# Kernel optimization log

Measured on AMD Instinct MI355X. Metric: run time of the kernel, lower is better.

Reference implementation:

```python
import jax, jax.numpy as jnp
import numpy as np

K_NN = 3
EPS = 1e-8
MASK_THRESH = 0.5


def _three_nn_interpolate(pts, known, feats):
    """pts: (B,N,3), known: (B,M,3), feats: (B,M,C) -> (B,N,C).
    Squared-distance 3-NN + inverse-distance weighted interpolation
    (pointnet2 three_nn / three_interpolate semantics)."""
    # (B,N,M) squared euclidean distances
    d2 = (jnp.sum(pts * pts, -1)[:, :, None]
          + jnp.sum(known * known, -1)[:, None, :]
          - 2.0 * jnp.einsum('bnd,bmd->bnm', pts, known))
    neg_d, idx = jax.lax.top_k(-d2, K_NN)          # (B,N,3)
    dist = jnp.maximum(-neg_d, 0.0)                # squared dists, clamp fp error
    dist_recip = 1.0 / (dist + EPS)
    weight = dist_recip / jnp.sum(dist_recip, -1, keepdims=True)  # (B,N,3)
    b_idx = jnp.arange(pts.shape[0])[:, None, None]
    gathered = feats[b_idx, idx]                   # (B,N,3,C)
    return jnp.sum(weight[..., None] * gathered, axis=2)  # (B,N,C)


def setup_inputs() -> dict:
    key = jax.random.key(0)
    ks = jax.random.split(key, 10)
    B, N, C = 4, 8192, 32
    M2, M3, M4, Mm = 8192, 4096, 2048, 4096
    sc = 10.0  # spread coords over a realistic metric range
    return {
        'points_mean': jax.random.normal(ks[0], (B, N, 3)) * sc,
        'known2': jax.random.normal(ks[1], (B, M2, 3)) * sc,
        'feats2': jax.random.normal(ks[2], (B, M2, C)),
        'known3': jax.random.normal(ks[3], (B, M3, 3)) * sc,
        'feats3': jax.random.normal(ks[4], (B, M3, C)),
        'known4': jax.random.normal(ks[5], (B, M4, 3)) * sc,
        'feats4': jax.random.normal(ks[6], (B, M4, C)),
        'match_points': jax.random.normal(ks[7], (B, Mm, 3)) * sc,
        'w_fc': jax.random.normal(ks[8], (64, 96)) * 0.1,
        'w_cls': jax.random.normal(ks[9], (1, 64)) * 0.1,
    }


def reference(points_mean, known2, feats2, known3, feats3, known4, feats4,
              match_points, w_fc, w_cls):
    p0 = _three_nn_interpolate(points_mean, known2, feats2)  # (B,N,32)
    p1 = _three_nn_interpolate(points_mean, known3, feats3)
    p2 = _three_nn_interpolate(points_mean, known4, feats4)
    pointwise = jnp.concatenate([p0, p1, p2], axis=-1) @ w_fc.T  # (B,N,64)
    pred_hm = pointwise @ w_cls.T                                 # (B,N,1)
    # GT mask: min distance to match points < 0.5 m
    d2 = (jnp.sum(points_mean * points_mean, -1)[:, :, None]
          + jnp.sum(match_points * match_points, -1)[:, None, :]
          - 2.0 * jnp.einsum('bnd,bmd->bnm', points_mean, match_points))
    min_d = jnp.sqrt(jnp.maximum(jnp.min(d2, axis=-1), 0.0))      # (B,N)
    gt_hm = (min_d < MASK_THRESH).astype(jnp.float32)
    return pred_hm, gt_hm
```

## Files before the change

kernel.cpp:

```cpp
#include <hip/hip_runtime.h>

typedef unsigned int u32;
typedef unsigned long long u64;
typedef float f32x2 __attribute__((ext_vector_type(2)));

#define NB 4
#define NQ 8192
#define MARGIN 0.0625f
#define NBKT 4096

#define OFF_C0   0u
#define OFF_C1   524288u
#define OFF_C2   786432u
#define OFF_CMP  917504u
#define OFF_SKEY 1179648u
#define OFF_BOX  2031616u
#define OFF_WV   2068480u
#define WS_NEW2  2068992u
#define OFF_CM   917504u
#define WS_OLD   (512u*1024 + 256u*1024 + 128u*1024 + 512u*1024)

struct __align__(32) CP { f32x2 x, y, z, w; };
struct DM { double x, y, z, w; };

__device__ __forceinline__ f32x2 fma2(f32x2 a, f32x2 b, f32x2 c) {
  return __builtin_elementwise_fma(a, b, c);
}

__device__ __forceinline__ void lexins(double& e0d, double& e1d, double& e2d,
                                       int& e0i, int& e1i, int& e2i,
                                       double d, int i) {
  if (d < e2d || (d == e2d && i < e2i)) {
    if (d < e0d || (d == e0d && i < e0i)) {
      e2d = e1d; e2i = e1i; e1d = e0d; e1i = e0i; e0d = d; e0i = i;
    } else if (d < e1d || (d == e1d && i < e1i)) {
      e2d = e1d; e2i = e1i; e1d = d; e1i = i;
    } else {
      e2d = d; e2i = i;
    }
  }
}

__device__ __forceinline__ void ins4(float kv, u32 idx,
                                     float& k0, float& k1, float& k2, float& k3,
                                     u32& i0, u32& i1, u32& i2, u32& i3) {
  if (kv < k3) {
    bool lt0 = kv < k0, lt1 = kv < k1, lt2 = kv < k2;
    k3 = lt2 ? k2 : kv;               i3 = lt2 ? i2 : idx;
    k2 = lt2 ? (lt1 ? k1 : kv) : k2;  i2 = lt2 ? (lt1 ? i1 : idx) : i2;
    k1 = lt1 ? (lt0 ? k0 : kv) : k1;  i1 = lt1 ? (lt0 ? i0 : idx) : i1;
    k0 = lt0 ? kv : k0;               i0 = lt0 ? idx : i0;
  }
}

__device__ __forceinline__ u32 spread10(u32 v) {
  v &= 0x3FFu;
  v = (v | (v << 16)) & 0x030000FFu;
  v = (v | (v << 8))  & 0x0300F00Fu;
  v = (v | (v << 4))  & 0x030C30C3u;
  v = (v | (v << 2))  & 0x09249249u;
  return v;
}
__device__ __forceinline__ u32 morton30(float x, float y, float z) {
  int xi = (int)((x + 64.f) * 8.f);
  int yi = (int)((y + 64.f) * 8.f);
  int zi = (int)((z + 64.f) * 8.f);
  xi = min(max(xi, 0), 1023); yi = min(max(yi, 0), 1023); zi = min(max(zi, 0), 1023);
  return spread10((u32)xi) | (spread10((u32)yi) << 1) | (spread10((u32)zi) << 2);
}

__device__ __forceinline__ size_t skey_abase(int arr) {
  return (arr == 0) ? 0 : (arr == 1) ? 32768 : (arr == 2) ? 49152
        : (arr == 3) ? 57344 : 73728;
}

__global__ __launch_bounds__(1024) void prep_csort(
    const float* __restrict__ k2p, const float* __restrict__ k3p,
    const float* __restrict__ k4p, const float* __restrict__ mmp,
    const float* __restrict__ pts, u64* __restrict__ skey) {
  __shared__ u32 hist[NBKT];
  __shared__ u32 wsum[16];
  const int arr = blockIdx.x, b = blockIdx.y, tid = threadIdx.x;
  const int lane = tid & 63, wv = tid >> 6;
  const float* src = (arr == 0) ? k2p : (arr == 1) ? k3p : (arr == 2) ? k4p
                      : (arr == 3) ? mmp : pts;
  const int n = (arr == 0) ? 8192 : (arr == 1) ? 4096 : (arr == 2) ? 2048
                 : (arr == 3) ? 4096 : 8192;
  const float* sb = src + (size_t)b * n * 3;
  u64* skb = skey + skey_abase(arr) + (size_t)b * n;

  for (int i = tid; i < NBKT; i += 1024) hist[i] = 0;
  __syncthreads();
  for (int i = tid; i < n; i += 1024) {
    u32 k = morton30(sb[3 * i], sb[3 * i + 1], sb[3 * i + 2]);
    atomicAdd(&hist[k >> 18], 1u);
  }
  __syncthreads();
  u32 h0 = hist[4 * tid], h1 = hist[4 * tid + 1];
  u32 h2 = hist[4 * tid + 2], h3 = hist[4 * tid + 3];
  u32 s4 = h0 + h1 + h2 + h3;
  u32 inc = s4;
#pragma unroll
  for (int o = 1; o < 64; o <<= 1) {
    u32 t = __shfl_up(inc, o);
    if (lane >= o) inc += t;
  }
  if (lane == 63) wsum[wv] = inc;
  __syncthreads();
  if (tid < 16) {
    u32 v = wsum[tid], in = v;
#pragma unroll
    for (int o = 1; o < 16; o <<= 1) {
      u32 t = __shfl_up(in, o);
      if (tid >= o) in += t;
    }
    wsum[tid] = in - v;
  }
  __syncthreads();
  u32 excl = wsum[wv] + (inc - s4);
  hist[4 * tid]     = excl;
  hist[4 * tid + 1] = excl + h0;
  hist[4 * tid + 2] = excl + h0 + h1;
  hist[4 * tid + 3] = excl + h0 + h1 + h2;
  __syncthreads();
  for (int i = tid; i < n; i += 1024) {
    u32 k = morton30(sb[3 * i], sb[3 * i + 1], sb[3 * i + 2]);
    u32 pos = atomicAdd(&hist[k >> 18], 1u);
    skb[pos] = ((u64)k << 32) | (u32)i;
  }
}

__global__ __launch_bounds__(512) void refine_emit(
    const float* __restrict__ k2p, const float* __restrict__ k3p,
    const float* __restrict__ k4p, const float* __restrict__ mmp,
    const float* __restrict__ pts, u64* __restrict__ skey,
    CP* __restrict__ c0, CP* __restrict__ c1, CP* __restrict__ c2,
    CP* __restrict__ cmp, float* __restrict__ boxes,
    const float* __restrict__ wfc, const float* __restrict__ wcls,
    float* __restrict__ wvg) {
  const int widx = blockIdx.x, b = blockIdx.y, tid = threadIdx.x;
  if (widx == 52) {
    if (b == 0 && tid < 96) {
      float acc = 0.f;
      for (int j = 0; j < 64; ++j) acc += wcls[j] * wfc[j * 96 + tid];
      wvg[tid] = acc;
    }
    return;
  }
  __shared__ u64 ex[512];
  int arr, win;
  if (widx < 16)      { arr = 0; win = widx; }
  else if (widx < 24) { arr = 1; win = widx - 16; }
  else if (widx < 28) { arr = 2; win = widx - 24; }
  else if (widx < 36) { arr = 3; win = widx - 28; }
  else                { arr = 4; win = widx - 36; }
  const float* src = (arr == 0) ? k2p : (arr == 1) ? k3p : (arr == 2) ? k4p
                      : (arr == 3) ? mmp : pts;
  const int n = (arr == 0) ? 8192 : (arr == 1) ? 4096 : (arr == 2) ? 2048
                 : (arr == 3) ? 4096 : 8192;
  u64* skb = skey + skey_abase(arr) + (size_t)b * n;
  const int e = win * 512 + tid;
  u64 v = skb[e];

  for (int k = 2; k <= 512; k <<= 1) {
    for (int j = k >> 1; j > 0; j >>= 1) {
      u64 w;
      if (j < 64) {
        w = __shfl_xor(v, j);
      } else {
        __syncthreads();
        ex[tid] = v;
        __syncthreads();
        w = ex[tid ^ j];
      }
      bool up = (tid & k) == 0;
      bool lower = (tid & j) == 0;
      v = (up == lower) ? (v < w ? v : w) : (v < w ? w : v);
    }
  }
  skb[e] = v;
  if (arr == 4) return;

  u32 p = (u32)v;
  const float* sb = src + (size_t)b * n * 3;
  float x = sb[3 * p], y = sb[3 * p + 1], z = sb[3 * p + 2];
  {
    CP* dst = (arr == 0) ? c0 : (arr == 1) ? c1 : (arr == 2) ? c2 : cmp;
    float* df = (float*)(dst + (size_t)b * (n >> 1) + (e >> 1));
    int sl = e & 1;
    df[sl]     = x;
    df[2 + sl] = y;
    df[4 + sl] = z;
    df[6 + sl] = fmaf(z, z, fmaf(y, y, x * x));
  }
  float xlo = x, xhi = x, ylo = y, yhi = y, zlo = z, zhi = z;
#pragma unroll
  for (int off = 1; off < 64; off <<= 1) {
    xlo = fminf(xlo, __shfl_xor(xlo, off)); xhi = fmaxf(xhi, __shfl_xor(xhi, off));
    ylo = fminf(ylo, __shfl_xor(ylo, off)); yhi = fmaxf(yhi, __shfl_xor(yhi, off));
    zlo = fminf(zlo, __shfl_xor(zlo, off)); zhi = fmaxf(zhi, __shfl_xor(zhi, off));
  }
  if ((tid & 63) == 0) {
    const int nG = n >> 6, g = e >> 6;
    const int boff = (arr == 0) ? 0 : (arr == 1) ? 512 : (arr == 2) ? 768 : 896;
    float* bx = boxes + ((size_t)boff + (size_t)b * nG + g) * 8;
    bx[0] = xlo; bx[1] = xhi; bx[2] = ylo; bx[3] = yhi; bx[4] = zlo; bx[5] = zhi;
    bx[6] = 0.f; bx[7] = 0.f;
  }
}

__device__ __forceinline__ void scan_pairs16(
    const CP* __restrict__ cg, u32 ebase,
    f32x2 mx2, f32x2 my2, f32x2 mz2,
    float& k0, float& k1, float& k2, float& k3,
    u32& i0, u32& i1, u32& i2, u32& i3) {
#pragma unroll 4
  for (int gg = 0; gg < 16; gg += 4) {
    f32x2 key[4];
#pragma unroll
    for (int u = 0; u < 4; ++u) {
      CP c = cg[gg + u];
      key[u] = fma2(mx2, c.x, fma2(my2, c.y, fma2(mz2, c.z, c.w)));
    }
#pragma unroll
    for (int u = 0; u < 4; ++u) {
      float ka = key[u].x, kb = key[u].y;
      if (fminf(ka, kb) < k3) {
        u32 ib = ebase + (u32)((gg + u) * 2);
        ins4(ka, ib,     k0, k1, k2, k3, i0, i1, i2, i3);
        ins4(kb, ib + 1, k0, k1, k2, k3, i0, i1, i2, i3);
      }
    }
  }
}

struct Smem4 {
  float  box[2304];
  float  qx[32], qy[32], qz[32];
  double qdx[32], qdy[32], qdz[32], qn[32];
  u32    oq[32];
  u32    di[3][32][4][4];
  double mmin[32][8];
  float  wv[96];
  float  wq[32][9];
  u32    iq[32][9];
  float  contrib[32][9];
  float4 stage[4][2][64];
  u32    list[4][64];
};

__global__ __launch_bounds__(256, 4) void fused_sorted3(
    const float* __restrict__ pts,
    const float* __restrict__ f2, const float* __restrict__ f3,
    const float* __restrict__ f4,
    const float* __restrict__ wvg,
    const CP* __restrict__ c0, const CP* __restrict__ c1,
    const CP* __restrict__ c2, const CP* __restrict__ cmp,
    const u64* __restrict__ skey, const float* __restrict__ boxes,
    float* __restrict__ out) {
  __shared__ Smem4 s;
  const int tid = threadIdx.x;
  const int b = blockIdx.y;
  const int tile = blockIdx.x;
  const int lane = tid & 63;
  const int q = tid & 31;
  const int h = (tid >> 5) & 1;
  const int wid = __builtin_amdgcn_readfirstlane(tid >> 6);

  for (int i = tid; i < 2304; i += 256) {
    int src;
    if (i < 1024)      src = (b * 128) * 8 + i;
    else if (i < 1536) src = (512 + b * 64) * 8 + (i - 1024);
    else if (i < 1792) src = (768 + b * 32) * 8 + (i - 1536);
    else               src = (896 + b * 64) * 8 + (i - 1792);
    s.box[i] = boxes[src];
  }
  if (tid < 32) {
    u64 kv = skey[73728 + (size_t)b * NQ + tile * 32 + tid];
    u32 p = (u32)kv;
    const float* pb = pts + (size_t)b * NQ * 3;
    float x = pb[3 * p], y = pb[3 * p + 1], z = pb[3 * p + 2];
    s.qx[tid] = x; s.qy[tid] = y; s.qz[tid] = z; s.oq[tid] = p;
    double dx = (double)x, dy = (double)y, dz = (double)z;
    s.qdx[tid] = dx; s.qdy[tid] = dy; s.qdz[tid] = dz;
    s.qn[tid] = (dx * dx + dy * dy) + dz * dz;
  } else if (tid < 128) {
    s.wv[tid - 32] = wvg[tid - 32];
  }
  __syncthreads();

  const float qx = s.qx[q], qy = s.qy[q], qz = s.qz[q];
  const float qnf = fmaf(qz, qz, fmaf(qy, qy, qx * qx));
  const float fm2x = -2.0f * qx, fm2y = -2.0f * qy, fm2z = -2.0f * qz;
  const double qdx = s.qdx[q], qdy = s.qdy[q], qdz = s.qdz[q], qn = s.qn[q];
  const f32x2 mx2 = {fm2x, fm2x}, my2 = {fm2y, fm2y}, mz2 = {fm2z, fm2z};

  {
    int lvl, part, nG, g0, stride, nvote, lboff;
    if (wid < 2)      { lvl = 0; nG = 128; stride = 2; nvote = 63;
                        g0 = (((tile * 128) >> 8) & ~1) | wid;
                        part = wid * 2 + h; lboff = 0; }
    else if (wid == 2){ lvl = 1; nG = 64;  stride = 1; nvote = 63;
                        g0 = (tile * 64) >> 8; part = h; lboff = 128; }
    else              { lvl = 2; nG = 32;  stride = 1; nvote = 31;
                        g0 = (tile * 32) >> 8; part = h; lboff = 192; }
    const int M = 8192 >> lvl;
    const CP* c4 = ((lvl == 0) ? c0 : ((lvl == 1) ? c1 : c2)) + (((size_t)b * M) >> 1);

    float k0 = __builtin_inff(), k1 = k0, k2 = k0, k3 = k0;
    u32 i0 = 0, i1 = 0, i2 = 0, i3 = 0;

    scan_pairs16(c4 + g0 * 32 + h * 16, (u32)(g0 * 64 + h * 32),
                 mx2, my2, mz2, k0, k1, k2, k3, i0, i1, i2, i3);

    int nl = 0;
    for (int t = 1; t <= nvote; ++t) {
      int g = (g0 + stride * t) & (nG - 1);
      const float* bx = &s.box[(lboff + g) * 8];
      float dx = fmaxf(fmaxf(bx[0] - qx, qx - bx[1]), 0.f);
      float dy = fmaxf(fmaxf(bx[2] - qy, qy - bx[3]), 0.f);
      float dz = fmaxf(fmaxf(bx[4] - qz, qz - bx[5]), 0.f);
      float lb = fmaf(dx, dx, fmaf(dy, dy, dz * dz));
      if (__any(lb < qnf + k3 + MARGIN)) {
        if (lane == 0) s.list[wid][nl] = (u32)g;
        ++nl;
      }
    }

    auto accept = [&](int g) -> bool {
      const float* bx = &s.box[(lboff + g) * 8];
      float dx = fmaxf(fmaxf(bx[0] - qx, qx - bx[1]), 0.f);
      float dy = fmaxf(fmaxf(bx[2] - qy, qy - bx[3]), 0.f);
      float dz = fmaxf(fmaxf(bx[4] - qz, qz - bx[5]), 0.f);
      float lb = fmaf(dx, dx, fmaf(dy, dy, dz * dz));
      return __any(lb < qnf + k3 + MARGIN);
    };
    int ip = 0, cur = 0, gcur = -1;
    float4 v;
    while (ip < nl) {
      int g = (int)s.list[wid][ip++];
      if (accept(g)) { gcur = g; v = ((const float4*)(c4 + (size_t)g * 32))[lane]; break; }
    }
    while (gcur >= 0) {
      s.stage[wid][cur][lane] = v;
      int gn = -1;
      while (ip < nl) {
        int g = (int)s.list[wid][ip++];
        if (accept(g)) { gn = g; break; }
      }
      if (gn >= 0) v = ((const float4*)(c4 + (size_t)gn * 32))[lane];
      const CP* sg = (const CP*)&s.stage[wid][cur][0];
      scan_pairs16(sg + h * 16, (u32)(gcur * 64 + h * 32),
                   mx2, my2, mz2, k0, k1, k2, k3, i0, i1, i2, i3);
      gcur = gn; cur ^= 1;
    }

    s.di[lvl][q][part][0] = i0; s.di[lvl][q][part][1] = i1;
    s.di[lvl][q][part][2] = i2; s.di[lvl][q][part][3] = i3;
  }

  {
    const CP* cmb = cmp + (size_t)b * 2048;
    int gm0 = tile >> 2;
    double dmin = __builtin_inf();
    for (int t = 0; t < 16; ++t) {
      int g = (gm0 + wid + 4 * t) & 63;
      const float* bx = &s.box[(224 + g) * 8];
      float dx = fmaxf(fmaxf(bx[0] - qx, qx - bx[1]), 0.f);
      float dy = fmaxf(fmaxf(bx[2] - qy, qy - bx[3]), 0.f);
      float dz = fmaxf(fmaxf(bx[4] - qz, qz - bx[5]), 0.f);
      float lb = fmaf(dx, dx, fmaf(dy, dy, dz * dz));
      if (__any(lb < 0.26f)) {
        const CP* cg = cmb + g * 32 + h * 16;
#pragma unroll 4
        for (int p = 0; p < 16; ++p) {
          CP c = cg[p];
          f32x2 key = fma2(mx2, c.x, fma2(my2, c.y, fma2(mz2, c.z, c.w)));
          if (fminf(key.x, key.y) + qnf < 0.252f) {
            {
              double x = (double)c.x.x, y = (double)c.y.x, z = (double)c.z.x;
              double kn2 = (x * x + y * y) + z * z;
              double dot = (qdx * x + qdy * y) + qdz * z;
              dmin = fmin(dmin, (qn + kn2) - 2.0 * dot);
            }
            {
              double x = (double)c.x.y, y = (double)c.y.y, z = (double)c.z.y;
              double kn2 = (x * x + y * y) + z * z;
              double dot = (qdx * x + qdy * y) + qdz * z;
              dmin = fmin(dmin, (qn + kn2) - 2.0 * dot);
            }
          }
        }
      }
    }
    s.mmin[q][wid * 2 + h] = dmin;
  }
  __syncthreads();

  const int gqbase = b * NQ;
  if (tid < 96) {
    const int lvl = tid >> 5;
    const int qq = tid & 31;
    const int M  = 8192 >> lvl;
    const int np = (lvl == 0) ? 4 : 2;
    const CP* c4 = ((lvl == 0) ? c0 : ((lvl == 1) ? c1 : c2)) + (((size_t)b * M) >> 1);
    const u64* skl = skey + ((lvl == 0) ? 0 : (lvl == 1) ? 32768 : 49152)
                     + (size_t)b * M;
    const double tqdx = s.qdx[qq], tqdy = s.qdy[qq], tqdz = s.qdz[qq], tqn = s.qn[qq];
    double e0 = __builtin_inf(), e1 = e0, e2 = e0;
    int j0 = 0, j1 = 0, j2 = 0;
    for (int hh = 0; hh < np; ++hh) {
#pragma unroll
      for (int r = 0; r < 4; ++r) {
        int sidx = (int)s.di[lvl][qq][hh][r];
        CP cc = c4[sidx >> 1];
        bool hi = sidx & 1;
        double x = (double)(hi ? cc.x.y : cc.x.x);
        double y = (double)(hi ? cc.y.y : cc.y.x);
        double z = (double)(hi ? cc.z.y : cc.z.x);
        int orig = (int)(u32)skl[sidx];
        double kn2 = (x * x + y * y) + z * z;
        double dot = (tqdx * x + tqdy * y) + tqdz * z;
        double d2 = (tqn + kn2) - 2.0 * dot;
        lexins(e0, e1, e2, j0, j1, j2, d2, orig);
      }
    }
    double d0 = fmax(e0, 0.0), d1 = fmax(e1, 0.0), d2v = fmax(e2, 0.0);
    double r0 = 1.0 / (d0 + 1e-8);
    double r1 = 1.0 / (d1 + 1e-8);
    double r2 = 1.0 / (d2v + 1e-8);
    double sum = (r0 + r1) + r2;
    s.wq[qq][lvl * 3 + 0] = (float)(r0 / sum); s.iq[qq][lvl * 3 + 0] = (u32)j0;
    s.wq[qq][lvl * 3 + 1] = (float)(r1 / sum); s.iq[qq][lvl * 3 + 1] = (u32)j1;
    s.wq[qq][lvl * 3 + 2] = (float)(r2 / sum); s.iq[qq][lvl * 3 + 2] = (u32)j2;
  } else if (tid < 128) {
    const int qq = tid - 96;
    double dm = s.mmin[qq][0];
#pragma unroll
    for (int p = 1; p < 8; ++p) dm = fmin(dm, s.mmin[qq][p]);
    out[NB * NQ + gqbase + (int)s.oq[qq]] = (dm < 0.25) ? 1.0f : 0.0f;
  }
  __syncthreads();

  for (int item = tid; item < 288; item += 256) {
    const int qq = item & 31, j = item >> 5;
    const int lvl = j / 3;
    const float* fp = (lvl == 0) ? f2 : ((lvl == 1) ? f3 : f4);
    const int M = 8192 >> lvl;
    const float4* row = (const float4*)(fp + ((size_t)b * M + s.iq[qq][j]) * 32);
    const float* wvp = s.wv + lvl * 32;
    float acc = 0.f;
#pragma unroll
    for (int v = 0; v < 8; ++v) {
      float4 r = row[v];
      acc += wvp[4 * v] * r.x + wvp[4 * v + 1] * r.y
           + wvp[4 * v + 2] * r.z + wvp[4 * v + 3] * r.w;
    }
    s.contrib[qq][j] = s.wq[qq][j] * acc;
  }
  __syncthreads();
  if (tid < 32) {
    const float* c = s.contrib[tid];
    float l0 = (c[0] + c[1]) + c[2];
    float l1 = (c[3] + c[4]) + c[5];
    float l2 = (c[6] + c[7]) + c[8];
    out[gqbase + (int)s.oq[tid]] = (l0 + l1) + l2;
  }
}

__global__ __launch_bounds__(256) void prep_kernel(
    const float* __restrict__ k2p, const float* __restrict__ k3p,
    const float* __restrict__ k4p, const float* __restrict__ mmp,
    CP* __restrict__ c0, CP* __restrict__ c1,
    CP* __restrict__ c2, DM* __restrict__ cm) {
  int r = blockIdx.y;
  int i = blockIdx.x * 256 + threadIdx.x;
  if (r < 3) {
    const float* src = (r == 0) ? k2p : ((r == 1) ? k3p : k4p);
    CP* dst = (r == 0) ? c0 : ((r == 1) ? c1 : c2);
    int pairs = (r == 0) ? NB * 4096 : ((r == 1) ? NB * 2048 : NB * 1024);
    if (i >= pairs) return;
    const float* p = src + (size_t)i * 6;
    float x0 = p[0], y0 = p[1], z0 = p[2];
    float x1 = p[3], y1 = p[4], z1 = p[5];
    CP c;
    c.x = f32x2{x0, x1}; c.y = f32x2{y0, y1}; c.z = f32x2{z0, z1};
    c.w = f32x2{fmaf(z0, z0, fmaf(y0, y0, x0 * x0)),
                fmaf(z1, z1, fmaf(y1, y1, x1 * x1))};
    dst[i] = c;
  } else {
    if (i >= NB * 4096) return;
    double x = (double)mmp[3 * i], y = (double)mmp[3 * i + 1], z = (double)mmp[3 * i + 2];
    DM d = {x, y, z, fma(z, z, fma(y, y, x * x))};
    cm[i] = d;
  }
}

template <bool PREP>
__device__ __forceinline__ void scan_nn(
    const CP* __restrict__ cp, const float* __restrict__ raw,
    int gstart, int L, float m2x, float m2y, float m2z,
    float* kk, u32* ii) {
  float k0 = __builtin_inff(), k1 = k0, k2 = k0, k3 = k0;
  u32 i0 = 0, i1 = 0, i2 = 0, i3 = 0;
  if (PREP) {
    const f32x2 mx2 = {m2x, m2x}, my2 = {m2y, m2y}, mz2 = {m2z, m2z};
    const int G = L >> 1;
#pragma unroll 2
    for (int g = 0; g < G; g += 4) {
      f32x2 key[4];
#pragma unroll
      for (int u = 0; u < 4; ++u) {
        CP c = cp[g + u];
        key[u] = fma2(mx2, c.x, fma2(my2, c.y, fma2(mz2, c.z, c.w)));
      }
#pragma unroll
      for (int u = 0; u < 4; ++u) {
        float ka = key[u].x, kb = key[u].y;
        if (fminf(ka, kb) < k3) {
          u32 ib = (u32)(gstart + 2 * (g + u));
          ins4(ka, ib,     k0, k1, k2, k3, i0, i1, i2, i3);
          ins4(kb, ib + 1, k0, k1, k2, k3, i0, i1, i2, i3);
        }
      }
    }
  } else {
    for (int j = 0; j < L; j += 8) {
      float key[8];
#pragma unroll
      for (int u = 0; u < 8; ++u) {
        const float* p = raw + (size_t)(gstart + j + u) * 3;
        float x = p[0], y = p[1], z = p[2];
        float n2 = fmaf(z, z, fmaf(y, y, x * x));
        key[u] = fmaf(m2x, x, fmaf(m2y, y, fmaf(m2z, z, n2)));
      }
#pragma unroll
      for (int u = 0; u < 8; ++u)
        ins4(key[u], (u32)(gstart + j + u), k0, k1, k2, k3, i0, i1, i2, i3);
    }
  }
  kk[0] = k0; kk[1] = k1; kk[2] = k2; kk[3] = k3;
  ii[0] = i0; ii[1] = i1; ii[2] = i2; ii[3] = i3;
}

template <bool PREP>
__device__ __forceinline__ double scan_mask(
    const DM* __restrict__ c8, const float* __restrict__ raw,
    int gstart, int L, double m2x, double m2y, double m2z) {
  double smin = __builtin_inf();
  if (PREP) {
    for (int j = 0; j < L; j += 8) {
      double sv[8];
#pragma unroll
      for (int u = 0; u < 8; ++u) {
        DM c = c8[gstart + j + u];
        sv[u] = fma(m2x, c.x, fma(m2y, c.y, fma(m2z, c.z, c.w)));
      }
      double m01 = fmin(sv[0], sv[1]), m23 = fmin(sv[2], sv[3]);
      double m45 = fmin(sv[4], sv[5]), m67 = fmin(sv[6], sv[7]);
      smin = fmin(smin, fmin(fmin(m01, m23), fmin(m45, m67)));
    }
  } else {
    for (int j = 0; j < L; j += 4) {
#pragma unroll
      for (int u = 0; u < 4; ++u) {
        const float* p = raw + (size_t)(gstart + j + u) * 3;
        double x = (double)p[0], y = (double)p[1], z = (double)p[2];
        double kn = fma(z, z, fma(y, y, x * x));
        smin = fmin(smin, fma(m2x, x, fma(m2y, y, fma(m2z, z, kn))));
      }
    }
  }
  return smin;
}

struct Smem {
  float  qx[64], qy[64], qz[64];
  double qdx[64], qdy[64], qdz[64], qn[64];
  float  dk[3][64][4][4];
  u32    di[3][64][4][4];
  double mmin[64][8];
  float  wv[96];
  float  part[64][3];
};

template <bool PREP>
__global__ __launch_bounds__(512, 2) void fused_kernel(
    const float* __restrict__ pts,
    const float* __restrict__ k2p, const float* __restrict__ f2,
    const float* __restrict__ k3p, const float* __restrict__ f3,
    const float* __restrict__ k4p, const float* __restrict__ f4,
    const float* __restrict__ mmp,
    const float* __restrict__ wfc, const float* __restrict__ wcls,
    const CP* __restrict__ c0, const CP* __restrict__ c1,
    const CP* __restrict__ c2, const DM* __restrict__ cm,
    float* __restrict__ out) {
  __shared__ Smem s;
  const int tid = threadIdx.x;
  const int b = blockIdx.y;
  const int q0 = blockIdx.x * 64;
  const int qloc = tid & 63;
  const int wid = __builtin_amdgcn_readfirstlane(tid >> 6);

  if (tid < 64) {
    int gq = b * NQ + q0 + tid;
    float x = pts[3 * gq], y = pts[3 * gq + 1], z = pts[3 * gq + 2];
    s.qx[tid] = x; s.qy[tid] = y; s.qz[tid] = z;
    double dx = (double)x, dy = (double)y, dz = (double)z;
    s.qdx[tid] = dx; s.qdy[tid] = dy; s.qdz[tid] = dz;
    s.qn[tid] = (dx * dx + dy * dy) + dz * dz;
  } else if (tid < 160) {
    int t = tid - 64;
    float acc = 0.f;
    for (int j = 0; j < 64; ++j) acc += wcls[j] * wfc[j * 96 + t];
    s.wv[t] = acc;
  }
  __syncthreads();

  const float fm2x = -2.0f * s.qx[qloc];
  const float fm2y = -2.0f * s.qy[qloc];
  const float fm2z = -2.0f * s.qz[qloc];
  const double dm2x = -2.0 * s.qdx[qloc];
  const double dm2y = -2.0 * s.qdy[qloc];
  const double dm2z = -2.0 * s.qdz[qloc];

  {
    int lvl, prt, gstart, glen;
    if (wid < 4)      { lvl = 0; prt = wid;     gstart = wid * 2048;       glen = 2048; }
    else if (wid < 6) { lvl = 1; prt = wid - 4; gstart = (wid - 4) * 2048; glen = 2048; }
    else              { lvl = 2; prt = wid - 6; gstart = (wid - 6) * 1024; glen = 1024; }
    const CP* c4 = (lvl == 0) ? c0 : ((lvl == 1) ? c1 : c2);
    const float* raw = (lvl == 0) ? k2p : ((lvl == 1) ? k3p : k4p);
    const int      M = (lvl == 0) ? 8192 : ((lvl == 1) ? 4096 : 2048);
    float kk[4]; u32 ii[4];
    scan_nn<PREP>(c4 + (PREP ? (((size_t)b * M + gstart) >> 1) : 0),
                  raw + (size_t)b * M * 3,
                  gstart, glen, fm2x, fm2y, fm2z, kk, ii);
#pragma unroll
    for (int r = 0; r < 4; ++r) {
      s.dk[lvl][qloc][prt][r] = kk[r];
      s.di[lvl][qloc][prt][r] = ii[r];
    }
    int mstart, mlen;
    if (wid < 6) { mstart = wid * 256; mlen = 256; }
    else         { mstart = 1536 + (wid - 6) * 1280; mlen = 1280; }
    s.mmin[qloc][wid] = scan_mask<PREP>(cm + (PREP ? (size_t)b * 4096 : 0),
                                        mmp + (size_t)b * 4096 * 3,
                                        mstart, mlen, dm2x, dm2y, dm2z);
  }
  __syncthreads();

  const int gqbase = b * NQ + q0;
  if (tid < 192) {
    const int lvl = __builtin_amdgcn_readfirstlane(tid >> 6);
    const int q = tid & 63;
    const float* kp = (lvl == 0) ? k2p : ((lvl == 1) ? k3p : k4p);
    const int    M  = (lvl == 0) ? 8192 : ((lvl == 1) ? 4096 : 2048);
    const int    np = (lvl == 0) ? 4 : 2;
    const double qdx = s.qdx[q], qdy = s.qdy[q], qdz = s.qdz[q], qn = s.qn[q];
    double e0 = __builtin_inf(), e1 = e0, e2 = e0;
    int i0 = 0, i1 = 0, i2 = 0;
    for (int h = 0; h < np; ++h) {
#pragma unroll
      for (int r = 0; r < 4; ++r) {
        int idx = (int)s.di[lvl][q][h][r];
        const float* c = kp + ((size_t)b * M + idx) * 3;
        double x = (double)c[0], y = (double)c[1], z = (double)c[2];
        double kn2 = (x * x + y * y) + z * z;
        double dot = (qdx * x + qdy * y) + qdz * z;
        double d2 = (qn + kn2) - 2.0 * dot;
        lexins(e0, e1, e2, i0, i1, i2, d2, idx);
      }
    }
    double d0 = fmax(e0, 0.0), d1 = fmax(e1, 0.0), d2v = fmax(e2, 0.0);
    double r0 = 1.0 / (d0 + 1e-8);
    double r1 = 1.0 / (d1 + 1e-8);
    double r2 = 1.0 / (d2v + 1e-8);
    double sum = (r0 + r1) + r2;
    float wa = (float)(r0 / sum), wb = (float)(r1 / sum), wc = (float)(r2 / sum);
    const float* fp = (lvl == 0) ? f2 : ((lvl == 1) ? f3 : f4);
    const float* g0 = fp + ((size_t)b * M + i0) * 32;
    const float* g1 = fp + ((size_t)b * M + i1) * 32;
    const float* g2 = fp + ((size_t)b * M + i2) * 32;
    float acc = 0.f;
#pragma unroll
    for (int wd = 0; wd < 32; ++wd) {
      float v = (wa * g0[wd] + wb * g1[wd]) + wc * g2[wd];
      acc += s.wv[lvl * 32 + wd] * v;
    }
    s.part[q][lvl] = acc;
  } else if (tid < 256) {
    const int q = tid - 192;
    double sm = s.mmin[q][0];
#pragma unroll
    for (int p = 1; p < 8; ++p) sm = fmin(sm, s.mmin[q][p]);
    double dm = s.qn[q] + sm;
    out[NB * NQ + gqbase + q] = (dm < 0.25) ? 1.0f : 0.0f;
  }
  __syncthreads();
  if (tid < 64) {
    float pred = (s.part[tid][0] + s.part[tid][1]) + s.part[tid][2];
    out[gqbase + tid] = pred;
  }
}

extern "C" void kernel_launch(void* const* d_in, const int* in_sizes, int n_in,
                              void* d_out, int out_size, void* d_ws, size_t ws_size,
                              hipStream_t stream) {
  const float* pts    = (const float*)d_in[0];
  const float* known2 = (const float*)d_in[1];
  const float* feats2 = (const float*)d_in[2];
  const float* known3 = (const float*)d_in[3];
  const float* feats3 = (const float*)d_in[4];
  const float* known4 = (const float*)d_in[5];
  const float* feats4 = (const float*)d_in[6];
  const float* match  = (const float*)d_in[7];
  const float* wfc    = (const float*)d_in[8];
  const float* wcls   = (const float*)d_in[9];

  char* ws = (char*)d_ws;
  CP* c0 = (CP*)(ws + OFF_C0);
  CP* c1 = (CP*)(ws + OFF_C1);
  CP* c2 = (CP*)(ws + OFF_C2);

  if (ws_size >= WS_NEW2) {
    CP* cmp = (CP*)(ws + OFF_CMP);
    u64* skey = (u64*)(ws + OFF_SKEY);
    float* boxes = (float*)(ws + OFF_BOX);
    float* wvg = (float*)(ws + OFF_WV);
    hipLaunchKernelGGL(prep_csort, dim3(5, NB), dim3(1024), 0, stream,
                       known2, known3, known4, match, pts, skey);
    hipLaunchKernelGGL(refine_emit, dim3(53, NB), dim3(512), 0, stream,
                       known2, known3, known4, match, pts, skey,
                       c0, c1, c2, cmp, boxes, wfc, wcls, wvg);
    hipLaunchKernelGGL(fused_sorted3, dim3(NQ / 32, NB), dim3(256), 0, stream,
                       pts, feats2, feats3, feats4, wvg,
                       c0, c1, c2, cmp, skey, boxes, (float*)d_out);
  } else if (ws_size >= WS_OLD) {
    DM* cm = (DM*)(ws + OFF_CM);
    hipLaunchKernelGGL(prep_kernel, dim3(64, 4), dim3(256), 0, stream,
                       known2, known3, known4, match, c0, c1, c2, cm);
    hipLaunchKernelGGL(HIP_KERNEL_NAME(fused_kernel<true>), dim3(NQ / 64, NB),
                       dim3(512), 0, stream, pts, known2, feats2, known3, feats3,
                       known4, feats4, match, wfc, wcls, c0, c1, c2, cm,
                       (float*)d_out);
  } else {
    DM* cm = (DM*)(ws + OFF_CM);
    hipLaunchKernelGGL(HIP_KERNEL_NAME(fused_kernel<false>), dim3(NQ / 64, NB),
                       dim3(512), 0, stream, pts, known2, feats2, known3, feats3,
                       known4, feats4, match, wfc, wcls, c0, c1, c2, cm,
                       (float*)d_out);
  }
}
```

Before: 224.5 us.

## Rebalance 3-NN search jobs across wavefronts with finer level partitions

Instead of assigning each wavefront one level (two to level 0, one each to levels 1 and 2), the search work is split into eight partitions: level 0 into 2 stride partitions, levels 1 and 2 into 4 each. The partitions are distributed so every wavefront handles a comparable share of work, aiming to cut the idle time of the wavefronts that finish early. Candidate indices are stored as 16-bit values so the larger per-query candidate table still fits in shared memory. The cost is that levels 1 and 2 now each merge 8 partial candidate lists instead of 2, and each extra partition repeats its home-group scan and box-vote loop.

After: 264.2 us. 17.7% more time.

```diff
diff --git a/kernel.cpp b/kernel.cpp
--- a/kernel.cpp
+++ b/kernel.cpp
@@ -2,6 +2,7 @@
 
 typedef unsigned int u32;
 typedef unsigned long long u64;
+typedef unsigned short u16;
 typedef float f32x2 __attribute__((ext_vector_type(2)));
 
 #define NB 4
@@ -234,12 +235,12 @@
   }
 }
 
-struct Smem4 {
+struct Smem8 {
   float  box[2304];
   float  qx[32], qy[32], qz[32];
   double qdx[32], qdy[32], qdz[32], qn[32];
   u32    oq[32];
-  u32    di[3][32][4][4];
+  u16    di[3][32][8][4];
   double mmin[32][8];
   float  wv[96];
   float  wq[32][9];
@@ -249,7 +250,7 @@
   u32    list[4][64];
 };
 
-__global__ __launch_bounds__(256, 4) void fused_sorted3(
+__global__ __launch_bounds__(256, 4) void fused_bal(
     const float* __restrict__ pts,
     const float* __restrict__ f2, const float* __restrict__ f3,
     const float* __restrict__ f4,
@@ -258,7 +259,7 @@
     const CP* __restrict__ c2, const CP* __restrict__ cmp,
     const u64* __restrict__ skey, const float* __restrict__ boxes,
     float* __restrict__ out) {
-  __shared__ Smem4 s;
+  __shared__ Smem8 s;
   const int tid = threadIdx.x;
   const int b = blockIdx.y;
   const int tile = blockIdx.x;
@@ -296,67 +297,82 @@
   const f32x2 mx2 = {fm2x, fm2x}, my2 = {fm2y, fm2y}, mz2 = {fm2z, fm2z};
 
   {
-    int lvl, part, nG, g0, stride, nvote, lboff;
-    if (wid < 2)      { lvl = 0; nG = 128; stride = 2; nvote = 63;
-                        g0 = (((tile * 128) >> 8) & ~1) | wid;
-                        part = wid * 2 + h; lboff = 0; }
-    else if (wid == 2){ lvl = 1; nG = 64;  stride = 1; nvote = 63;
-                        g0 = (tile * 64) >> 8; part = h; lboff = 128; }
-    else              { lvl = 2; nG = 32;  stride = 1; nvote = 31;
-                        g0 = (tile * 32) >> 8; part = h; lboff = 192; }
-    const int M = 8192 >> lvl;
-    const CP* c4 = ((lvl == 0) ? c0 : ((lvl == 1) ? c1 : c2)) + (((size_t)b * M) >> 1);
-
-    float k0 = __builtin_inff(), k1 = k0, k2 = k0, k3 = k0;
-    u32 i0 = 0, i1 = 0, i2 = 0, i3 = 0;
-
-    scan_pairs16(c4 + g0 * 32 + h * 16, (u32)(g0 * 64 + h * 32),
-                 mx2, my2, mz2, k0, k1, k2, k3, i0, i1, i2, i3);
-
-    int nl = 0;
-    for (int t = 1; t <= nvote; ++t) {
-      int g = (g0 + stride * t) & (nG - 1);
-      const float* bx = &s.box[(lboff + g) * 8];
-      float dx = fmaxf(fmaxf(bx[0] - qx, qx - bx[1]), 0.f);
-      float dy = fmaxf(fmaxf(bx[2] - qy, qy - bx[3]), 0.f);
-      float dz = fmaxf(fmaxf(bx[4] - qz, qz - bx[5]), 0.f);
-      float lb = fmaf(dx, dx, fmaf(dy, dy, dz * dz));
-      if (__any(lb < qnf + k3 + MARGIN)) {
-        if (lane == 0) s.list[wid][nl] = (u32)g;
-        ++nl;
-      }
-    }
-
-    auto accept = [&](int g) -> bool {
-      const float* bx = &s.box[(lboff + g) * 8];
-      float dx = fmaxf(fmaxf(bx[0] - qx, qx - bx[1]), 0.f);
-      float dy = fmaxf(fmaxf(bx[2] - qy, qy - bx[3]), 0.f);
-      float dz = fmaxf(fmaxf(bx[4] - qz, qz - bx[5]), 0.f);
-      float lb = fmaf(dx, dx, fmaf(dy, dy, dz * dz));
-      return __any(lb < qnf + k3 + MARGIN);
-    };
-    int ip = 0, cur = 0, gcur = -1;
-    float4 v;
-    while (ip < nl) {
-      int g = (int)s.list[wid][ip++];
-      if (accept(g)) { gcur = g; v = ((const float4*)(c4 + (size_t)g * 32))[lane]; break; }
-    }
-    while (gcur >= 0) {
-      s.stage[wid][cur][lane] = v;
-      int gn = -1;
+    int jlvl[3] = {-1, -1, -1}, jpar[3] = {0, 0, 0}, jPP[3] = {2, 2, 2};
+    if (wid == 0)      { jlvl[0] = 0; jpar[0] = 0; jPP[0] = 2;
+                         jlvl[1] = 1; jpar[1] = 0; jPP[1] = 4; }
+    else if (wid == 1) { jlvl[0] = 0; jpar[0] = 1; jPP[0] = 2;
+                         jlvl[1] = 2; jpar[1] = 0; jPP[1] = 4; }
+    else if (wid == 2) { jlvl[0] = 1; jpar[0] = 1; jPP[0] = 4;
+                         jlvl[1] = 1; jpar[1] = 2; jPP[1] = 4;
+                         jlvl[2] = 2; jpar[2] = 1; jPP[2] = 4; }
+    else               { jlvl[0] = 1; jpar[0] = 3; jPP[0] = 4;
+                         jlvl[1] = 2; jpar[1] = 2; jPP[1] = 4;
+                         jlvl[2] = 2; jpar[2] = 3; jPP[2] = 4; }
+#pragma unroll
+    for (int jj = 0; jj < 3; ++jj) {
+      const int lvl = jlvl[jj];
+      if (lvl < 0) break;
+      const int par = jpar[jj], P = jPP[jj];
+      const int M = 8192 >> lvl;
+      const int nG = M >> 6;
+      const int lboff = (lvl == 0) ? 0 : ((lvl == 1) ? 128 : 192);
+      const CP* c4 = ((lvl == 0) ? c0 : ((lvl == 1) ? c1 : c2)) + (((size_t)b * M) >> 1);
+      const int home = (lvl == 0) ? (tile >> 1) : ((lvl == 1) ? (tile >> 2) : (tile >> 3));
+      const int g0 = (home & ~(P - 1)) | par;
+
+      float k0 = __builtin_inff(), k1 = k0, k2 = k0, k3 = k0;
+      u32 i0 = 0, i1 = 0, i2 = 0, i3 = 0;
+
+      scan_pairs16(c4 + g0 * 32 + h * 16, (u32)(g0 * 64 + h * 32),
+                   mx2, my2, mz2, k0, k1, k2, k3, i0, i1, i2, i3);
+
+      int nl = 0;
+      const int nvote = nG / P - 1;
+      for (int t = 1; t <= nvote; ++t) {
+        int g = (g0 + P * t) & (nG - 1);
+        const float* bx = &s.box[(lboff + g) * 8];
+        float dx = fmaxf(fmaxf(bx[0] - qx, qx - bx[1]), 0.f);
+        float dy = fmaxf(fmaxf(bx[2] - qy, qy - bx[3]), 0.f);
+        float dz = fmaxf(fmaxf(bx[4] - qz, qz - bx[5]), 0.f);
+        float lb = fmaf(dx, dx, fmaf(dy, dy, dz * dz));
+        if (__any(lb < qnf + k3 + MARGIN)) {
+          if (lane == 0) s.list[wid][nl] = (u32)g;
+          ++nl;
+        }
+      }
+
+      auto accept = [&](int g) -> bool {
+        const float* bx = &s.box[(lboff + g) * 8];
+        float dx = fmaxf(fmaxf(bx[0] - qx, qx - bx[1]), 0.f);
+        float dy = fmaxf(fmaxf(bx[2] - qy, qy - bx[3]), 0.f);
+        float dz = fmaxf(fmaxf(bx[4] - qz, qz - bx[5]), 0.f);
+        float lb = fmaf(dx, dx, fmaf(dy, dy, dz * dz));
+        return __any(lb < qnf + k3 + MARGIN);
+      };
+      int ip = 0, cur = 0, gcur = -1;
+      float4 v;
       while (ip < nl) {
         int g = (int)s.list[wid][ip++];
-        if (accept(g)) { gn = g; break; }
-      }
-      if (gn >= 0) v = ((const float4*)(c4 + (size_t)gn * 32))[lane];
-      const CP* sg = (const CP*)&s.stage[wid][cur][0];
-      scan_pairs16(sg + h * 16, (u32)(gcur * 64 + h * 32),
-                   mx2, my2, mz2, k0, k1, k2, k3, i0, i1, i2, i3);
-      gcur = gn; cur ^= 1;
-    }
-
-    s.di[lvl][q][part][0] = i0; s.di[lvl][q][part][1] = i1;
-    s.di[lvl][q][part][2] = i2; s.di[lvl][q][part][3] = i3;
+        if (accept(g)) { gcur = g; v = ((const float4*)(c4 + (size_t)g * 32))[lane]; break; }
+      }
+      while (gcur >= 0) {
+        s.stage[wid][cur][lane] = v;
+        int gn = -1;
+        while (ip < nl) {
+          int g = (int)s.list[wid][ip++];
+          if (accept(g)) { gn = g; break; }
+        }
+        if (gn >= 0) v = ((const float4*)(c4 + (size_t)gn * 32))[lane];
+        const CP* sg = (const CP*)&s.stage[wid][cur][0];
+        scan_pairs16(sg + h * 16, (u32)(gcur * 64 + h * 32),
+                     mx2, my2, mz2, k0, k1, k2, k3, i0, i1, i2, i3);
+        gcur = gn; cur ^= 1;
+      }
+
+      const int part = par * 2 + h;
+      s.di[lvl][q][part][0] = (u16)i0; s.di[lvl][q][part][1] = (u16)i1;
+      s.di[lvl][q][part][2] = (u16)i2; s.di[lvl][q][part][3] = (u16)i3;
+    }
   }
 
   {
@@ -402,7 +418,7 @@
     const int lvl = tid >> 5;
     const int qq = tid & 31;
     const int M  = 8192 >> lvl;
-    const int np = (lvl == 0) ? 4 : 2;
+    const int np = (lvl == 0) ? 4 : 8;
     const CP* c4 = ((lvl == 0) ? c0 : ((lvl == 1) ? c1 : c2)) + (((size_t)b * M) >> 1);
     const u64* skl = skey + ((lvl == 0) ? 0 : (lvl == 1) ? 32768 : 49152)
                      + (size_t)b * M;
@@ -733,7 +749,7 @@
     hipLaunchKernelGGL(refine_emit, dim3(53, NB), dim3(512), 0, stream,
                        known2, known3, known4, match, pts, skey,
                        c0, c1, c2, cmp, boxes, wfc, wcls, wvg);
-    hipLaunchKernelGGL(fused_sorted3, dim3(NQ / 32, NB), dim3(256), 0, stream,
+    hipLaunchKernelGGL(fused_bal, dim3(NQ / 32, NB), dim3(256), 0, stream,
                        pts, feats2, feats3, feats4, wvg,
                        c0, c1, c2, cmp, skey, boxes, (float*)d_out);
   } else if (ws_size >= WS_OLD) {
```
